# Performance work log

Measured on AMD Instinct MI355X. Metric: run time of the kernel, lower is better.

The kernel has to match this reference:

```python
import jax, jax.numpy as jnp
import numpy as np

H, S, B, R, IN, NN, OP = 512, 256, 32, 16, 4, 16, 6
NEG = -1.0e12


def setup_inputs() -> dict:
    key = jax.random.key(0)
    ks = jax.random.split(key, 40)
    f32 = jnp.float32
    inp = {}
    inp["node_emb"] = jax.random.normal(ks[0], (B, 1, H), f32)
    inp["left"] = jax.random.normal(ks[1], (B, 1, H), f32)
    inp["encoder_outputs"] = jax.random.normal(ks[2], (S, B, H), f32)
    inp["num_pades"] = jax.random.normal(ks[3], (B, NN, H), f32)
    inp["formula_scores"] = jax.random.normal(ks[4], (R, H), f32)
    inp["has_left"] = jax.random.bernoulli(ks[5], 0.5, (B,))
    lengths = jax.random.randint(ks[6], (B,), S // 2, S + 1)
    inp["seq_mask"] = jnp.arange(S)[None, :] >= lengths[:, None]
    nlen = jax.random.randint(ks[7], (B,), (IN + NN) // 2, IN + NN + 1)
    inp["mask_nums"] = jnp.arange(IN + NN)[None, :] >= nlen[:, None]
    sc = 0.04  # init scale for weights
    def w(i, shape):
        return jax.random.normal(ks[i], shape, f32) * sc
    inp["embedding_weight"] = jax.random.normal(ks[8], (1, IN, H), f32)
    inp["Wcl"] = w(9, (H, H));    inp["bcl"] = jnp.zeros((H,), f32)
    inp["Wclg"] = w(10, (H, H));  inp["bclg"] = jnp.zeros((H,), f32)
    inp["Wcr"] = w(11, (2 * H, H));  inp["bcr"] = jnp.zeros((H,), f32)
    inp["Wcrg"] = w(12, (2 * H, H)); inp["bcrg"] = jnp.zeros((H,), f32)
    inp["Wops"] = w(13, (2 * H, OP)); inp["bops"] = jnp.zeros((OP,), f32)
    inp["Wattn"] = w(14, (2 * H, H)); inp["battn"] = jnp.zeros((H,), f32)
    inp["wattn_s"] = w(15, (H,));     inp["battn_s"] = jnp.zeros((), f32)
    inp["Wfattn"] = w(16, (2 * H, H)); inp["bfattn"] = jnp.zeros((H,), f32)
    inp["wfattn_s"] = w(17, (H,));     inp["bfattn_s"] = jnp.zeros((), f32)
    inp["Wscore"] = w(18, (3 * H, H)); inp["bscore"] = jnp.zeros((H,), f32)
    inp["wscore_s"] = w(19, (H,))  # Score.score has no bias
    inp["Wfp1"] = w(20, (H, H));   inp["bfp1"] = jnp.zeros((H,), f32)
    inp["Wfp2"] = w(21, (H,));     inp["bfp2"] = jnp.zeros((), f32)
    return inp


def _forward(node_emb, left, has_left, encoder_outputs, num_pades, seq_mask,
             mask_nums, formula_scores, embedding_weight, Wcl, bcl, Wclg, bclg,
             Wcr, bcr, Wcrg, bcrg, Wops, bops, Wattn, battn, wattn_s, battn_s,
             Wfattn, bfattn, wfattn_s, bfattn_s, Wscore, bscore, wscore_s,
             Wfp1, bfp1, Wfp2, bfp2):
    # gated left/right node update (dropout = identity, eval mode)
    c = node_emb                                            # [B,1,H]
    lc = jnp.concatenate([left, c], axis=-1)                # [B,1,2H]
    out_l = jnp.tanh(c @ Wcl + bcl) * jax.nn.sigmoid(c @ Wclg + bclg)
    out_r = jnp.tanh(lc @ Wcr + bcr) * jax.nn.sigmoid(lc @ Wcrg + bcrg)
    current_node = jnp.where(has_left[:, None, None], out_r, out_l)  # [B,1,H]
    # TreeAttn(current_node, encoder_outputs): additive attention over S
    Wh, We = Wattn[:H], Wattn[H:]
    feat = jnp.tanh(current_node[:, 0][None] @ Wh + encoder_outputs @ We + battn)  # [S,B,H]
    en = (feat @ wattn_s + battn_s).T                       # [B,S]
    en = jnp.where(seq_mask, NEG, en)
    current_attn = jax.nn.softmax(en, axis=1)[:, None, :]   # [B,1,S]
    eo_b = jnp.transpose(encoder_outputs, (1, 0, 2))        # [B,S,H]
    current_context = current_attn @ eo_b                   # [B,1,H]
    # embedding table = learned constants + numbers from the problem
    emb_w = jnp.concatenate(
        [jnp.broadcast_to(embedding_weight, (node_emb.shape[0], IN, H)), num_pades], axis=1)  # [B,IN+NN,H]
    leaf_input = jnp.concatenate([current_node, current_context], axis=2)[:, 0]  # [B,2H]
    # FormulaAttn: additive attention of each formula over all tokens
    Wfe, Wff = Wfattn[:H], Wfattn[H:]
    ffeat = jnp.tanh(encoder_outputs[None] @ Wfe
                     + (formula_scores @ Wff)[:, None, None, :] + bfattn)  # [R,S,B,H]
    fen = jnp.transpose(ffeat @ wfattn_s + bfattn_s, (2, 0, 1))            # [B,R,S]
    fen = jnp.where(seq_mask[:, None, :], NEG, fen)
    formulas_attn = jax.nn.softmax(fen, axis=-1)            # [B,R,S]
    formulas_context = (formulas_attn + 0.2 * current_attn) @ eo_b         # [B,R,H]
    formula_feat = jnp.tanh(formulas_context @ Wfp1 + bfp1)
    formula_prob = jax.nn.softmax(formula_feat @ Wfp2 + bfp2, axis=-1)     # [B,R]
    # Score over candidate number embeddings
    N = IN + NN
    hid = jnp.broadcast_to(leaf_input[:, None, :], (leaf_input.shape[0], N, 2 * H))
    ein = jnp.concatenate([hid, emb_w], axis=-1)            # [B,N,3H]
    ns = jnp.tanh(ein @ Wscore + bscore) @ wscore_s         # [B,N]
    num_score = jnp.where(mask_nums, NEG, ns)
    op = leaf_input @ Wops + bops                           # [B,OP]
    return (num_score, op, current_node, current_context, emb_w, formula_prob)


def reference(node_emb, left, has_left, encoder_outputs, num_pades, seq_mask,
              mask_nums, formula_scores, embedding_weight, Wcl, bcl, Wclg, bclg,
              Wcr, bcr, Wcrg, bcrg, Wops, bops, Wattn, battn, wattn_s, battn_s,
              Wfattn, bfattn, wfattn_s, bfattn_s, Wscore, bscore, wscore_s,
              Wfp1, bfp1, Wfp2, bfp2):
    return _forward(node_emb, left, has_left, encoder_outputs, num_pades,
                    seq_mask, mask_nums, formula_scores, embedding_weight,
                    Wcl, bcl, Wclg, bclg, Wcr, bcr, Wcrg, bcrg, Wops, bops,
                    Wattn, battn, wattn_s, battn_s, Wfattn, bfattn, wfattn_s,
                    bfattn_s, Wscore, bscore, wscore_s, Wfp1, bfp1, Wfp2, bfp2)
```

## Files before the change

### kernel.cpp

```cpp
#include <hip/hip_runtime.h>
#include <hip/hip_bf16.h>
#include <stdint.h>

#define H 512
#define S 256
#define B 32
#define R 16
#define NEG -1000000000000.0f

typedef unsigned short u16;
typedef short short8 __attribute__((ext_vector_type(8)));
typedef float f32x4 __attribute__((ext_vector_type(4)));

__device__ __forceinline__ float bf2f(u16 u) {
  unsigned int v = ((unsigned int)u) << 16;
  float f; __builtin_memcpy(&f, &v, 4); return f;
}
__device__ __forceinline__ u16 f2u(float x) {
  __hip_bfloat16 h = __float2bfloat16(x);
  u16 u; __builtin_memcpy(&u, &h, 2); return u;
}
__device__ __forceinline__ float ftanh(float x) {
  float e = __expf(2.f * x);
  return 1.f - 2.f * __builtin_amdgcn_rcpf(e + 1.f);
}
__device__ __forceinline__ float fsig(float x) {
  return __builtin_amdgcn_rcpf(1.f + __expf(-x));
}
__device__ __forceinline__ void gload16(const void* g, void* l) {
  __builtin_amdgcn_global_load_lds(
      (const __attribute__((address_space(1))) unsigned int*)g,
      (__attribute__((address_space(3))) unsigned int*)l, 16, 0, 0);
}

__device__ __forceinline__ void trans_tile(const float* __restrict__ src, int nb, int k0,
                                           u16* __restrict__ dst, int n0, int Krows,
                                           float (*tile)[65], int t) {
  #pragma unroll
  for (int it = 0; it < 16; ++it) {
    int f = it * 256 + t; int r = f >> 6, c = f & 63;
    tile[r][c] = src[(size_t)(k0 + r) * 512 + nb + c];
  }
  __syncthreads();
  #pragma unroll
  for (int it = 0; it < 16; ++it) {
    int f = it * 256 + t; int r = f >> 6, c = f & 63;
    dst[(size_t)(n0 + r) * Krows + k0 + c] = f2u(tile[c][r]);
  }
}

__global__ __launch_bounds__(256) void k_prep1(
    const float* __restrict__ enc, u16* __restrict__ encb,
    const float* __restrict__ Wattn, const float* __restrict__ Wfattn, u16* __restrict__ Wt,
    const float* __restrict__ Wscore, u16* __restrict__ Wt2f,
    const float* __restrict__ Wfp1, u16* __restrict__ Wt3,
    u16* __restrict__ Wt4,
    const float* __restrict__ node_emb, const float* __restrict__ left,
    const int* __restrict__ has_left,
    const float* __restrict__ Wcl, const float* __restrict__ Wclg,
    const float* __restrict__ Wcr, const float* __restrict__ Wcrg,
    float* __restrict__ gp1, float* __restrict__ gp2,
    const float* __restrict__ emb_w, const float* __restrict__ num_pades,
    float* __restrict__ out_embw, u16* __restrict__ einb) {
  __shared__ float tile[64][65];
  __shared__ float x[128];
  int id = blockIdx.x, t = threadIdx.x;
  if (id < 2048) {
    int i = (id * 256 + t) * 8;
    float4 a = *(const float4*)(enc + i);
    float4 b = *(const float4*)(enc + i + 4);
    short8 o;
    o[0] = (short)f2u(a.x); o[1] = (short)f2u(a.y); o[2] = (short)f2u(a.z); o[3] = (short)f2u(a.w);
    o[4] = (short)f2u(b.x); o[5] = (short)f2u(b.y); o[6] = (short)f2u(b.z); o[7] = (short)f2u(b.w);
    *(short8*)(encb + i) = o;
  } else if (id < 2176) {
    int f = id - 2048; int gx = f & 15, gy = f >> 4;
    int n0 = gx * 64, k0 = gy * 64;
    const float* src = (n0 < 512) ? (Wattn + 512 * 512) : Wfattn;
    int nb = (n0 < 512) ? n0 : n0 - 512;
    trans_tile(src, nb, k0, Wt, n0, 512, tile, t);
  } else if (id < 2368) {
    int f = id - 2176; int gx = f & 7, gy = f >> 3;
    trans_tile(Wscore, gx * 64, gy * 64, Wt2f, gx * 64, 1536, tile, t);
  } else if (id < 2432) {
    int f = id - 2368; int gx = f & 7, gy = f >> 3;
    trans_tile(Wfp1, gx * 64, gy * 64, Wt3, gx * 64, 512, tile, t);
  } else if (id < 2560) {
    int f = id - 2432; int gx = f & 15, gy = f >> 4;
    int n0 = gx * 64, k0 = gy * 64;
    const float* src = (n0 < 512) ? Wattn : (Wfattn + 512 * 512);
    int nb = (n0 < 512) ? n0 : n0 - 512;
    trans_tile(src, nb, k0, Wt4, n0, 512, tile, t);
  } else if (id < 2816) {
    int f = id - 2560;
    int b = f >> 3, kc = f & 7;
    int hl = has_left[b];
    int k0 = kc * 128;
    float* o1 = gp1 + ((size_t)b * 8 + kc) * 512;
    float* o2 = gp2 + ((size_t)b * 8 + kc) * 512;
    if (!hl && kc >= 4) { o1[t] = 0.f; o1[t + 256] = 0.f; o2[t] = 0.f; o2[t + 256] = 0.f; return; }
    if (t < 128) {
      int k = k0 + t;
      x[t] = hl ? (k < 512 ? left[b * 512 + k] : node_emb[b * 512 + k - 512])
                : node_emb[b * 512 + k];
    }
    __syncthreads();
    const float* W1 = hl ? Wcr : Wcl;
    const float* W2 = hl ? Wcrg : Wclg;
    float a1 = 0.f, a2 = 0.f, a3 = 0.f, a4 = 0.f;
    for (int kk = 0; kk < 128; ++kk) {
      float xv = x[kk];
      const float* w1r = W1 + (size_t)(k0 + kk) * 512;
      const float* w2r = W2 + (size_t)(k0 + kk) * 512;
      a1 += xv * w1r[t]; a2 += xv * w1r[t + 256];
      a3 += xv * w2r[t]; a4 += xv * w2r[t + 256];
    }
    o1[t] = a1; o1[t + 256] = a2; o2[t] = a3; o2[t + 256] = a4;
  } else {
    int f = id - 2816;
    #pragma unroll
    for (int rr = 0; rr < 2; ++rr) {
      int row = f * 2 + rr;
      int n = row % 20, b = row / 20;
      #pragma unroll
      for (int i = 0; i < 2; ++i) {
        int h = t + 256 * i;
        float v = (n < 4) ? emb_w[n * 512 + h] : num_pades[((size_t)b * 16 + n - 4) * 512 + h];
        out_embw[(size_t)row * 512 + h] = v;
        einb[(size_t)row * 1536 + 1024 + h] = f2u(v);
      }
    }
  }
}

template <int FM, int FN>
__device__ __forceinline__ void gemm_body(
    const u16* __restrict__ A, const u16* __restrict__ Bt,
    u16* __restrict__ C16, float* __restrict__ C32,
    int lda, int ldb, int ldc, int ksteps,
    int bm, int bn, int kbase, long zoff,
    u16* As, u16* Bs) {
  constexpr int BM = FM * 32, BN = FN * 32;
  const int tid = threadIdx.x;
  const int lane = tid & 63;
  const int wid = tid >> 6;
  const int wr = (wid >> 1) * (FM * 16);
  const int wc = (wid & 1) * (FN * 16);
  f32x4 acc[FM][FN];
  #pragma unroll
  for (int m = 0; m < FM; ++m)
    #pragma unroll
    for (int n = 0; n < FN; ++n)
      #pragma unroll
      for (int q = 0; q < 4; ++q) acc[m][n][q] = 0.f;

  const int kb = (lane >> 4) * 8;
  const int rr = lane & 15;
  for (int ks = 0; ks < ksteps; ++ks) {
    int k0 = kbase + ks * 32;
    #pragma unroll
    for (int it = 0; it < BM / 64; ++it) {
      int c = it * 256 + tid;
      gload16(A + (size_t)(bm + (c >> 2)) * lda + k0 + (c & 3) * 8, As + c * 8);
    }
    #pragma unroll
    for (int it = 0; it < BN / 64; ++it) {
      int c = it * 256 + tid;
      gload16(Bt + (size_t)(bn + (c >> 2)) * ldb + k0 + (c & 3) * 8, Bs + c * 8);
    }
    __syncthreads();
    short8 af[FM], bf[FN];
    #pragma unroll
    for (int m = 0; m < FM; ++m)
      af[m] = *(const short8*)(As + (wr + m * 16 + rr) * 32 + kb);
    #pragma unroll
    for (int n = 0; n < FN; ++n)
      bf[n] = *(const short8*)(Bs + (wc + n * 16 + rr) * 32 + kb);
    #pragma unroll
    for (int m = 0; m < FM; ++m)
      #pragma unroll
      for (int n = 0; n < FN; ++n)
        acc[m][n] = __builtin_amdgcn_mfma_f32_16x16x32_bf16(af[m], bf[n], acc[m][n], 0, 0, 0);
    __syncthreads();
  }
  int r0 = (lane >> 4) * 4, cc = lane & 15;
  #pragma unroll
  for (int m = 0; m < FM; ++m)
    #pragma unroll
    for (int n = 0; n < FN; ++n)
      #pragma unroll
      for (int q = 0; q < 4; ++q) {
        long row = bm + wr + m * 16 + r0 + q;
        long col = bn + wc + n * 16 + cc;
        if (C16) C16[zoff + row * ldc + col] = f2u(acc[m][n][q]);
        else     C32[zoff + row * ldc + col] = acc[m][n][q];
      }
}

__global__ __launch_bounds__(256) void k_g1(
    const u16* __restrict__ encb, const u16* __restrict__ Wt, u16* __restrict__ EW,
    const u16* __restrict__ cnfs, const u16* __restrict__ Wt4, float* __restrict__ CWFW) {
  __shared__ u16 As[128 * 32];
  __shared__ u16 Bs[128 * 32];
  int x = blockIdx.x, y = blockIdx.y;
  if (x < 64)
    gemm_body<4, 4>(encb, Wt, EW, nullptr, 512, 512, 1024, 16, x * 128, y * 128, 0, 0, As, Bs);
  else
    gemm_body<4, 4>(cnfs, Wt4, nullptr, CWFW, 512, 512, 1024, 16, 0, y * 128, 0, 0, As, Bs);
}

__global__ __launch_bounds__(256) void k_tt(
    const u16* __restrict__ einb, const u16* __restrict__ Wt2f, float* __restrict__ Tp,
    const u16* __restrict__ fctxb, const u16* __restrict__ Wt3, float* __restrict__ T3p) {
  __shared__ u16 As[64 * 32];
  __shared__ u16 Bs[64 * 32];
  int q = blockIdx.x;
  if (q < 640) {
    int x = q % 10, y = (q / 10) % 8, z = q / 80;
    gemm_body<2, 2>(einb, Wt2f, nullptr, Tp, 1536, 1536, 512, 6,
                    x * 64, y * 64, z * 6 * 32, (long)z * 327680, As, Bs);
  } else {
    int q2 = q - 640;
    int x = q2 % 8, y = (q2 / 8) % 8, z = q2 / 64;
    gemm_body<2, 2>(fctxb, Wt3, nullptr, T3p, 512, 512, 512, 4,
                    x * 64, y * 64, z * 4 * 32, (long)z * 262144, As, Bs);
  }
}

__global__ __launch_bounds__(256) void k_p2(
    const float* __restrict__ gp1, const float* __restrict__ gp2,
    const int* __restrict__ has_left,
    const float* __restrict__ bcl, const float* __restrict__ bclg,
    const float* __restrict__ bcr, const float* __restrict__ bcrg,
    const float* __restrict__ fs,
    float* __restrict__ cur_node, float* __restrict__ out_cn, u16* __restrict__ cnfs) {
  int id = blockIdx.x, t = threadIdx.x;
  if (id < 32) {
    int b = id, hl = has_left[b];
    #pragma unroll
    for (int i = 0; i < 2; ++i) {
      int h = t + 256 * i;
      float s1 = 0.f, s2 = 0.f;
      #pragma unroll
      for (int c = 0; c < 8; ++c) {
        s1 += gp1[((size_t)b * 8 + c) * 512 + h];
        s2 += gp2[((size_t)b * 8 + c) * 512 + h];
      }
      float v = ftanh(s1 + (hl ? bcr[h] : bcl[h])) * fsig(s2 + (hl ? bcrg[h] : bclg[h]));
      cur_node[b * 512 + h] = v;
      out_cn[b * 512 + h] = v;
      cnfs[b * 512 + h] = f2u(v);
    }
  } else if (id < 48) {
    int r = id - 32;
    #pragma unroll
    for (int i = 0; i < 2; ++i) {
      int h = t + 256 * i;
      cnfs[id * 512 + h] = f2u(fs[r * 512 + h]);
    }
  } else {
    #pragma unroll
    for (int i = 0; i < 2; ++i) cnfs[id * 512 + t + 256 * i] = 0;
  }
}

__global__ __launch_bounds__(256) void k_enfen(
    const u16* __restrict__ EW, const float* __restrict__ CWFW,
    const float* __restrict__ battn, const float* __restrict__ bfattn,
    const float* __restrict__ wattn_s, const float* __restrict__ battn_s,
    const float* __restrict__ wfattn_s, const float* __restrict__ bfattn_s,
    const int* __restrict__ seq_mask, float* __restrict__ en, float* __restrict__ fen) {
  __shared__ float sFW[16 * 512];
  __shared__ float swf[512], swa[512], scw[512];
  int bid = blockIdx.x;
  int b = bid >> 6;
  int s0 = (bid & 63) * 4;
  int t = threadIdx.x;
  #pragma unroll
  for (int q = 0; q < 32; ++q) {
    int flat = q * 256 + t;
    int r = flat >> 9, h = flat & 511;
    sFW[flat] = CWFW[(size_t)(32 + r) * 1024 + 512 + h] + bfattn[h];
  }
  swf[t] = wfattn_s[t]; swf[256 + t] = wfattn_s[256 + t];
  swa[t] = wattn_s[t];  swa[256 + t] = wattn_s[256 + t];
  scw[t] = CWFW[(size_t)b * 1024 + t] + battn[t];
  scw[256 + t] = CWFW[(size_t)b * 1024 + 256 + t] + battn[256 + t];
  __syncthreads();
  int w = t >> 6, lane = t & 63;
  int s = s0 + w;
  const u16* ew = EW + (size_t)(s * 32 + b) * 1024;
  float ewf[8], wfv[8];
  float accE = 0.f;
  #pragma unroll
  for (int i = 0; i < 8; ++i) {
    int h = lane + 64 * i;
    accE += ftanh(scw[h] + bf2f(ew[h])) * swa[h];
    ewf[i] = bf2f(ew[512 + h]);
    wfv[i] = swf[h];
  }
  for (int o = 32; o >= 1; o >>= 1) accE += __shfl_down(accE, o);
  int msk = seq_mask[b * 256 + s];
  if (lane == 0) en[b * 256 + s] = msk ? NEG : (accE + battn_s[0]);
  for (int r = 0; r < 16; ++r) {
    float a = 0.f;
    #pragma unroll
    for (int i = 0; i < 8; ++i) {
      int h = lane + 64 * i;
      a += ftanh(sFW[r * 512 + h] + ewf[i]) * wfv[i];
    }
    for (int o = 32; o >= 1; o >>= 1) a += __shfl_down(a, o);
    if (lane == 0) fen[((size_t)b * 16 + r) * 256 + s] = msk ? NEG : (a + bfattn_s[0]);
  }
}

__global__ __launch_bounds__(512) void k_ctxall(
    const float* __restrict__ en, const float* __restrict__ fen,
    const u16* __restrict__ encb, const float* __restrict__ cur_node,
    float* __restrict__ out_ctx, float* __restrict__ leaf, u16* __restrict__ fctxb,
    u16* __restrict__ einb) {
  int br = blockIdx.x;
  int b = br / 17, j = br % 17;
  int t = threadIdx.x;
  __shared__ float red[512];
  __shared__ float sa[256];
  float xe = (t < 256) ? en[b * 256 + t] : NEG;
  red[t] = xe; __syncthreads();
  for (int o = 256; o > 0; o >>= 1) { if (t < o) red[t] = fmaxf(red[t], red[t + o]); __syncthreads(); }
  float m = red[0]; __syncthreads();
  float ee = (t < 256) ? __expf(xe - m) : 0.f;
  red[t] = ee; __syncthreads();
  for (int o = 256; o > 0; o >>= 1) { if (t < o) red[t] += red[t + o]; __syncthreads(); }
  float attn_v = ee / red[0];
  __syncthreads();
  float coef = attn_v;
  if (j < 16) {
    float xf = (t < 256) ? fen[((size_t)b * 16 + j) * 256 + t] : NEG;
    red[t] = xf; __syncthreads();
    for (int o = 256; o > 0; o >>= 1) { if (t < o) red[t] = fmaxf(red[t], red[t + o]); __syncthreads(); }
    float mf = red[0]; __syncthreads();
    float ef = (t < 256) ? __expf(xf - mf) : 0.f;
    red[t] = ef; __syncthreads();
    for (int o = 256; o > 0; o >>= 1) { if (t < o) red[t] += red[t + o]; __syncthreads(); }
    coef = ef / red[0] + 0.2f * attn_v;
    __syncthreads();
  }
  if (t < 256) sa[t] = coef;
  __syncthreads();
  int h = t;
  float acc = 0.f;
  #pragma unroll 8
  for (int s = 0; s < 256; ++s)
    acc += sa[s] * bf2f(encb[((size_t)s * 32 + b) * 512 + h]);
  if (j < 16) {
    fctxb[((size_t)b * 16 + j) * 512 + h] = f2u(acc);
  } else {
    float cn = cur_node[b * 512 + h];
    out_ctx[b * 512 + h] = acc;
    leaf[b * 1024 + 512 + h] = acc;
    leaf[b * 1024 + h] = cn;
    u16 v1 = f2u(cn), v2 = f2u(acc);
    for (int n = 0; n < 20; ++n) {
      einb[(size_t)(b * 20 + n) * 1536 + h] = v1;
      einb[(size_t)(b * 20 + n) * 1536 + 512 + h] = v2;
    }
  }
}

__global__ __launch_bounds__(256) void k_epi(
    const float* __restrict__ Tp, const float* __restrict__ bscore,
    const float* __restrict__ wscore_s, const int* __restrict__ mask_nums,
    float* __restrict__ out_ns,
    const float* __restrict__ T3p, const float* __restrict__ bfp1,
    const float* __restrict__ Wfp2, const float* __restrict__ bfp2,
    float* __restrict__ out_fp,
    const float* __restrict__ leaf, const float* __restrict__ Wops,
    const float* __restrict__ bops, float* __restrict__ out_op) {
  int id = blockIdx.x, t = threadIdx.x;
  int w = t >> 6, lane = t & 63;
  __shared__ float red[16];
  if (id < 640) {
    int row = id;
    float acc = 0.f;
    #pragma unroll
    for (int i = 0; i < 2; ++i) {
      int h = t + 256 * i;
      float tv = bscore[h];
      #pragma unroll
      for (int z = 0; z < 8; ++z) tv += Tp[(size_t)z * 327680 + (size_t)row * 512 + h];
      acc += ftanh(tv) * wscore_s[h];
    }
    for (int o = 32; o >= 1; o >>= 1) acc += __shfl_down(acc, o);
    if (lane == 0) red[w] = acc;
    __syncthreads();
    if (t == 0) out_ns[row] = mask_nums[row] ? NEG : (red[0] + red[1] + red[2] + red[3]);
  } else if (id < 672) {
    int b = id - 640;
    #pragma unroll
    for (int j2 = 0; j2 < 4; ++j2) {
      int j = w * 4 + j2;
      int row = b * 16 + j;
      float acc = 0.f;
      #pragma unroll
      for (int i = 0; i < 8; ++i) {
        int h = lane + 64 * i;
        float v = bfp1[h];
        #pragma unroll
        for (int z = 0; z < 4; ++z) v += T3p[(size_t)z * 262144 + (size_t)row * 512 + h];
        acc += ftanh(v) * Wfp2[h];
      }
      for (int o = 32; o >= 1; o >>= 1) acc += __shfl_down(acc, o);
      if (lane == 0) red[j] = acc + bfp2[0];
    }
    __syncthreads();
    if (t < 16) {
      float xx = red[t];
      float mm = xx;
      for (int o = 8; o >= 1; o >>= 1) mm = fmaxf(mm, __shfl_xor(mm, o, 16));
      float e = __expf(xx - mm);
      float s2 = e;
      for (int o = 8; o >= 1; o >>= 1) s2 += __shfl_xor(s2, o, 16);
      out_fp[b * 16 + t] = e / s2;
    }
  } else {
    int f = id - 672; int o = f % 6, b = f / 6;
    float acc = 0.f;
    #pragma unroll
    for (int i = 0; i < 4; ++i) {
      int k = t + 256 * i;
      acc += leaf[b * 1024 + k] * Wops[(size_t)k * 6 + o];
    }
    for (int off = 32; off >= 1; off >>= 1) acc += __shfl_down(acc, off);
    if (lane == 0) red[w] = acc;
    __syncthreads();
    if (t == 0) out_op[b * 6 + o] = red[0] + red[1] + red[2] + red[3] + bops[o];
  }
}

extern "C" void kernel_launch(void* const* d_in, const int* in_sizes, int n_in,
                              void* d_out, int out_size, void* d_ws, size_t ws_size,
                              hipStream_t stream) {
  const float* node_emb  = (const float*)d_in[0];
  const float* left      = (const float*)d_in[1];
  const float* enc       = (const float*)d_in[2];
  const float* num_pades = (const float*)d_in[3];
  const float* fs        = (const float*)d_in[4];
  const int*   has_left  = (const int*)d_in[5];
  const int*   seq_mask  = (const int*)d_in[6];
  const int*   mask_nums = (const int*)d_in[7];
  const float* emb_w     = (const float*)d_in[8];
  const float* Wcl  = (const float*)d_in[9];
  const float* bcl  = (const float*)d_in[10];
  const float* Wclg = (const float*)d_in[11];
  const float* bclg = (const float*)d_in[12];
  const float* Wcr  = (const float*)d_in[13];
  const float* bcr  = (const float*)d_in[14];
  const float* Wcrg = (const float*)d_in[15];
  const float* bcrg = (const float*)d_in[16];
  const float* Wops = (const float*)d_in[17];
  const float* bops = (const float*)d_in[18];
  const float* Wattn   = (const float*)d_in[19];
  const float* battn   = (const float*)d_in[20];
  const float* wattn_s = (const float*)d_in[21];
  const float* battn_s = (const float*)d_in[22];
  const float* Wfattn   = (const float*)d_in[23];
  const float* bfattn   = (const float*)d_in[24];
  const float* wfattn_s = (const float*)d_in[25];
  const float* bfattn_s = (const float*)d_in[26];
  const float* Wscore   = (const float*)d_in[27];
  const float* bscore   = (const float*)d_in[28];
  const float* wscore_s = (const float*)d_in[29];
  const float* Wfp1 = (const float*)d_in[30];
  const float* bfp1 = (const float*)d_in[31];
  const float* Wfp2 = (const float*)d_in[32];
  const float* bfp2 = (const float*)d_in[33];

  float* out = (float*)d_out;
  float* out_ns   = out + 0;
  float* out_op   = out + 640;
  float* out_cn   = out + 832;
  float* out_ctx  = out + 17216;
  float* out_embw = out + 33600;
  float* out_fp   = out + 361280;

  uint8_t* wsb = (uint8_t*)d_ws;
  u16*   encb = (u16*)(wsb + 0);
  u16*   Wt   = (u16*)(wsb + 8388608);
  u16*   Wt2f = (u16*)(wsb + 9437184);
  u16*   Wt3  = (u16*)(wsb + 11010048);
  u16*   Wt4  = (u16*)(wsb + 11534336);
  u16*   EW   = (u16*)(wsb + 12582912);
  u16*   einb = (u16*)(wsb + 29360128);
  u16*   cnfs = (u16*)(wsb + 31326208);
  float* CWFW = (float*)(wsb + 31457280);
  float* Tp   = (float*)(wsb + 31981568);
  float* T3p  = (float*)(wsb + 42467328);
  float* fb   = (float*)(wsb + 46661632);
  float* cur_node = fb + 0;
  float* en   = fb + 16384;
  float* fen  = fb + 24576;
  float* leaf = fb + 155648;
  u16*   fctxb= (u16*)(fb + 188416);
  float* gp1  = fb + 319488;
  float* gp2  = fb + 450560;

  k_prep1<<<3136, 256, 0, stream>>>(enc, encb, Wattn, Wfattn, Wt, Wscore, Wt2f, Wfp1, Wt3, Wt4,
                                    node_emb, left, has_left, Wcl, Wclg, Wcr, Wcrg,
                                    gp1, gp2, emb_w, num_pades, out_embw, einb);
  k_p2<<<128, 256, 0, stream>>>(gp1, gp2, has_left, bcl, bclg, bcr, bcrg, fs,
                                cur_node, out_cn, cnfs);
  k_g1<<<dim3(65, 8), 256, 0, stream>>>(encb, Wt, EW, cnfs, Wt4, CWFW);
  k_enfen<<<2048, 256, 0, stream>>>(EW, CWFW, battn, bfattn, wattn_s, battn_s,
                                    wfattn_s, bfattn_s, seq_mask, en, fen);
  k_ctxall<<<544, 512, 0, stream>>>(en, fen, encb, cur_node, out_ctx, leaf, fctxb, einb);
  k_tt<<<896, 256, 0, stream>>>(einb, Wt2f, Tp, fctxb, Wt3, T3p);
  k_epi<<<864, 256, 0, stream>>>(Tp, bscore, wscore_s, mask_nums, out_ns,
                                 T3p, bfp1, Wfp2, bfp2, out_fp,
                                 leaf, Wops, bops, out_op);
}
```

Measured before the change: 115.7 us.

## Split score GEMM into per-batch leaf term and per-node embedding term

```diff
diff --git a/kernel.cpp b/kernel.cpp
--- a/kernel.cpp
+++ b/kernel.cpp
@@ -52,7 +52,7 @@
 __global__ __launch_bounds__(256) void k_prep1(
     const float* __restrict__ enc, u16* __restrict__ encb,
     const float* __restrict__ Wattn, const float* __restrict__ Wfattn, u16* __restrict__ Wt,
-    const float* __restrict__ Wscore, u16* __restrict__ Wt2f,
+    const float* __restrict__ Wscore, u16* __restrict__ Wt2a, u16* __restrict__ Wt2b,
     const float* __restrict__ Wfp1, u16* __restrict__ Wt3,
     u16* __restrict__ Wt4,
     const float* __restrict__ node_emb, const float* __restrict__ left,
@@ -61,7 +61,7 @@
     const float* __restrict__ Wcr, const float* __restrict__ Wcrg,
     float* __restrict__ gp1, float* __restrict__ gp2,
     const float* __restrict__ emb_w, const float* __restrict__ num_pades,
-    float* __restrict__ out_embw, u16* __restrict__ einb) {
+    float* __restrict__ out_embw, u16* __restrict__ embb, u16* __restrict__ leafb) {
   __shared__ float tile[64][65];
   __shared__ float x[128];
   int id = blockIdx.x, t = threadIdx.x;
@@ -79,9 +79,12 @@
     const float* src = (n0 < 512) ? (Wattn + 512 * 512) : Wfattn;
     int nb = (n0 < 512) ? n0 : n0 - 512;
     trans_tile(src, nb, k0, Wt, n0, 512, tile, t);
+  } else if (id < 2240) {
+    int f = id - 2176; int gx = f & 7, gy = f >> 3;
+    trans_tile(Wscore + 1024 * 512, gx * 64, gy * 64, Wt2a, gx * 64, 512, tile, t);
   } else if (id < 2368) {
-    int f = id - 2176; int gx = f & 7, gy = f >> 3;
-    trans_tile(Wscore, gx * 64, gy * 64, Wt2f, gx * 64, 1536, tile, t);
+    int f = id - 2240; int gx = f & 7, gy = f >> 3;
+    trans_tile(Wscore, gx * 64, gy * 64, Wt2b, gx * 64, 1024, tile, t);
   } else if (id < 2432) {
     int f = id - 2368; int gx = f & 7, gy = f >> 3;
     trans_tile(Wfp1, gx * 64, gy * 64, Wt3, gx * 64, 512, tile, t);
@@ -116,7 +119,7 @@
       a3 += xv * w2r[t]; a4 += xv * w2r[t + 256];
     }
     o1[t] = a1; o1[t + 256] = a2; o2[t] = a3; o2[t + 256] = a4;
-  } else {
+  } else if (id < 3136) {
     int f = id - 2816;
     #pragma unroll
     for (int rr = 0; rr < 2; ++rr) {
@@ -127,9 +130,15 @@
         int h = t + 256 * i;
         float v = (n < 4) ? emb_w[n * 512 + h] : num_pades[((size_t)b * 16 + n - 4) * 512 + h];
         out_embw[(size_t)row * 512 + h] = v;
-        einb[(size_t)row * 1536 + 1024 + h] = f2u(v);
+        embb[(size_t)row * 512 + h] = f2u(v);
       }
     }
+  } else {
+    int f = id - 3136;
+    int base = 32 * 1024 + (f * 256 + t) * 16;
+    short8 z8 = {0,0,0,0,0,0,0,0};
+    *(short8*)(leafb + base) = z8;
+    *(short8*)(leafb + base + 8) = z8;
   }
 }
 
@@ -210,17 +219,22 @@
 }
 
 __global__ __launch_bounds__(256) void k_tt(
-    const u16* __restrict__ einb, const u16* __restrict__ Wt2f, float* __restrict__ Tp,
+    const u16* __restrict__ embb, const u16* __restrict__ Wt2a, float* __restrict__ Tep,
+    const u16* __restrict__ leafb, const u16* __restrict__ Wt2b, float* __restrict__ Tlp,
     const u16* __restrict__ fctxb, const u16* __restrict__ Wt3, float* __restrict__ T3p) {
   __shared__ u16 As[64 * 32];
   __shared__ u16 Bs[64 * 32];
   int q = blockIdx.x;
-  if (q < 640) {
+  if (q < 320) {
     int x = q % 10, y = (q / 10) % 8, z = q / 80;
-    gemm_body<2, 2>(einb, Wt2f, nullptr, Tp, 1536, 1536, 512, 6,
-                    x * 64, y * 64, z * 6 * 32, (long)z * 327680, As, Bs);
+    gemm_body<2, 2>(embb, Wt2a, nullptr, Tep, 512, 512, 512, 4,
+                    x * 64, y * 64, z * 4 * 32, (long)z * 327680, As, Bs);
+  } else if (q < 352) {
+    int q2 = q - 320; int y = q2 % 8, z = q2 / 8;
+    gemm_body<2, 2>(leafb, Wt2b, nullptr, Tlp, 1024, 1024, 512, 8,
+                    0, y * 64, z * 8 * 32, (long)z * 32768, As, Bs);
   } else {
-    int q2 = q - 640;
+    int q2 = q - 352;
     int x = q2 % 8, y = (q2 / 8) % 8, z = q2 / 64;
     gemm_body<2, 2>(fctxb, Wt3, nullptr, T3p, 512, 512, 512, 4,
                     x * 64, y * 64, z * 4 * 32, (long)z * 262144, As, Bs);
@@ -289,6 +303,14 @@
   __syncthreads();
   int w = t >> 6, lane = t & 63;
   int s = s0 + w;
+  int msk = seq_mask[b * 256 + s];
+  if (msk) {
+    if (lane == 0) {
+      en[b * 256 + s] = NEG;
+      for (int r = 0; r < 16; ++r) fen[((size_t)b * 16 + r) * 256 + s] = NEG;
+    }
+    return;
+  }
   const u16* ew = EW + (size_t)(s * 32 + b) * 1024;
   float ewf[8], wfv[8];
   float accE = 0.f;
@@ -300,8 +322,7 @@
     wfv[i] = swf[h];
   }
   for (int o = 32; o >= 1; o >>= 1) accE += __shfl_down(accE, o);
-  int msk = seq_mask[b * 256 + s];
-  if (lane == 0) en[b * 256 + s] = msk ? NEG : (accE + battn_s[0]);
+  if (lane == 0) en[b * 256 + s] = accE + battn_s[0];
   for (int r = 0; r < 16; ++r) {
     float a = 0.f;
     #pragma unroll
@@ -310,7 +331,7 @@
       a += ftanh(sFW[r * 512 + h] + ewf[i]) * wfv[i];
     }
     for (int o = 32; o >= 1; o >>= 1) a += __shfl_down(a, o);
-    if (lane == 0) fen[((size_t)b * 16 + r) * 256 + s] = msk ? NEG : (a + bfattn_s[0]);
+    if (lane == 0) fen[((size_t)b * 16 + r) * 256 + s] = a + bfattn_s[0];
   }
 }
 
@@ -318,7 +339,7 @@
     const float* __restrict__ en, const float* __restrict__ fen,
     const u16* __restrict__ encb, const float* __restrict__ cur_node,
     float* __restrict__ out_ctx, float* __restrict__ leaf, u16* __restrict__ fctxb,
-    u16* __restrict__ einb) {
+    u16* __restrict__ leafb) {
   int br = blockIdx.x;
   int b = br / 17, j = br % 17;
   int t = threadIdx.x;
@@ -359,16 +380,14 @@
     out_ctx[b * 512 + h] = acc;
     leaf[b * 1024 + 512 + h] = acc;
     leaf[b * 1024 + h] = cn;
-    u16 v1 = f2u(cn), v2 = f2u(acc);
-    for (int n = 0; n < 20; ++n) {
-      einb[(size_t)(b * 20 + n) * 1536 + h] = v1;
-      einb[(size_t)(b * 20 + n) * 1536 + 512 + h] = v2;
-    }
+    leafb[b * 1024 + h] = f2u(cn);
+    leafb[b * 1024 + 512 + h] = f2u(acc);
   }
 }
 
 __global__ __launch_bounds__(256) void k_epi(
-    const float* __restrict__ Tp, const float* __restrict__ bscore,
+    const float* __restrict__ Tep, const float* __restrict__ Tlp,
+    const float* __restrict__ bscore,
     const float* __restrict__ wscore_s, const int* __restrict__ mask_nums,
     float* __restrict__ out_ns,
     const float* __restrict__ T3p, const float* __restrict__ bfp1,
@@ -381,13 +400,16 @@
   __shared__ float red[16];
   if (id < 640) {
     int row = id;
+    int b = row / 20;
     float acc = 0.f;
     #pragma unroll
     for (int i = 0; i < 2; ++i) {
       int h = t + 256 * i;
       float tv = bscore[h];
       #pragma unroll
-      for (int z = 0; z < 8; ++z) tv += Tp[(size_t)z * 327680 + (size_t)row * 512 + h];
+      for (int z = 0; z < 4; ++z) tv += Tep[(size_t)z * 327680 + (size_t)row * 512 + h];
+      #pragma unroll
+      for (int z = 0; z < 4; ++z) tv += Tlp[(size_t)z * 32768 + (size_t)b * 512 + h];
       acc += ftanh(tv) * wscore_s[h];
     }
     for (int o = 32; o >= 1; o >>= 1) acc += __shfl_down(acc, o);
@@ -486,16 +508,19 @@
   uint8_t* wsb = (uint8_t*)d_ws;
   u16*   encb = (u16*)(wsb + 0);
   u16*   Wt   = (u16*)(wsb + 8388608);
-  u16*   Wt2f = (u16*)(wsb + 9437184);
+  u16*   Wt2a = (u16*)(wsb + 9437184);
+  u16*   Wt2b = (u16*)(wsb + 9961472);
   u16*   Wt3  = (u16*)(wsb + 11010048);
   u16*   Wt4  = (u16*)(wsb + 11534336);
   u16*   EW   = (u16*)(wsb + 12582912);
-  u16*   einb = (u16*)(wsb + 29360128);
-  u16*   cnfs = (u16*)(wsb + 31326208);
-  float* CWFW = (float*)(wsb + 31457280);
-  float* Tp   = (float*)(wsb + 31981568);
-  float* T3p  = (float*)(wsb + 42467328);
-  float* fb   = (float*)(wsb + 46661632);
+  u16*   embb = (u16*)(wsb + 29360128);
+  u16*   leafb= (u16*)(wsb + 30015488);
+  u16*   cnfs = (u16*)(wsb + 30146560);
+  float* CWFW = (float*)(wsb + 30277632);
+  float* Tep  = (float*)(wsb + 30801920);
+  float* Tlp  = (float*)(wsb + 36044800);
+  float* T3p  = (float*)(wsb + 36569088);
+  float* fb   = (float*)(wsb + 40763392);
   float* cur_node = fb + 0;
   float* en   = fb + 16384;
   float* fen  = fb + 24576;
@@ -504,17 +529,18 @@
   float* gp1  = fb + 319488;
   float* gp2  = fb + 450560;
 
-  k_prep1<<<3136, 256, 0, stream>>>(enc, encb, Wattn, Wfattn, Wt, Wscore, Wt2f, Wfp1, Wt3, Wt4,
+  k_prep1<<<3144, 256, 0, stream>>>(enc, encb, Wattn, Wfattn, Wt, Wscore, Wt2a, Wt2b,
+                                    Wfp1, Wt3, Wt4,
                                     node_emb, left, has_left, Wcl, Wclg, Wcr, Wcrg,
-                                    gp1, gp2, emb_w, num_pades, out_embw, einb);
+                                    gp1, gp2, emb_w, num_pades, out_embw, embb, leafb);
   k_p2<<<128, 256, 0, stream>>>(gp1, gp2, has_left, bcl, bclg, bcr, bcrg, fs,
                                 cur_node, out_cn, cnfs);
   k_g1<<<dim3(65, 8), 256, 0, stream>>>(encb, Wt, EW, cnfs, Wt4, CWFW);
   k_enfen<<<2048, 256, 0, stream>>>(EW, CWFW, battn, bfattn, wattn_s, battn_s,
                                     wfattn_s, bfattn_s, seq_mask, en, fen);
-  k_ctxall<<<544, 512, 0, stream>>>(en, fen, encb, cur_node, out_ctx, leaf, fctxb, einb);
-  k_tt<<<896, 256, 0, stream>>>(einb, Wt2f, Tp, fctxb, Wt3, T3p);
-  k_epi<<<864, 256, 0, stream>>>(Tp, bscore, wscore_s, mask_nums, out_ns,
+  k_ctxall<<<544, 512, 0, stream>>>(en, fen, encb, cur_node, out_ctx, leaf, fctxb, leafb);
+  k_tt<<<608, 256, 0, stream>>>(embb, Wt2a, Tep, leafb, Wt2b, Tlp, fctxb, Wt3, T3p);
+  k_epi<<<864, 256, 0, stream>>>(Tep, Tlp, bscore, wscore_s, mask_nums, out_ns,
                                  T3p, bfp1, Wfp2, bfp2, out_fp,
                                  leaf, Wops, bops, out_op);
 }
```

Measured after the change: 112.7 us. 2.6% less time.
